# Kernel tuning notes

Measured on AMD Instinct MI355X. Metric: run time of the kernel, lower is better.

The kernel has to match this reference:

```python
import jax, jax.numpy as jnp
import numpy as np

DIM = 2048
N_HEADS = 16
HEAD_DIM = DIM // N_HEADS

def setup_inputs() -> dict:
    key = jax.random.key(0)
    kx, kqkv, kout = jax.random.split(key, 3)
    x = jax.random.normal(kx, (2, 2048, DIM), dtype=jnp.float32)
    # nn.Linear weights stored [out_features, in_features]; y = x @ W.T
    W_qkv = jax.random.normal(kqkv, (3 * DIM, DIM), dtype=jnp.float32) * (DIM ** -0.5)
    W_out = jax.random.normal(kout, (DIM, DIM), dtype=jnp.float32) * (DIM ** -0.5)
    return {"x": x, "W_qkv": W_qkv, "W_out": W_out}

def reference(x, W_qkv, W_out):
    B, T, D = x.shape
    qkv = jnp.einsum('btd,ed->bte', x, W_qkv)  # [B,T,3D]
    q, k, v = jnp.split(qkv, 3, axis=-1)
    def heads(t):
        return t.reshape(B, T, N_HEADS, HEAD_DIM).transpose(0, 2, 1, 3)  # [B,H,T,d]
    q, k, v = heads(q), heads(k), heads(v)
    att = jnp.einsum('bhid,bhjd->bhij', q, k) / (HEAD_DIM ** 0.5)
    causal = jnp.tril(jnp.ones((T, T), dtype=bool))
    att = jnp.where(causal, att, -jnp.inf)
    att = jax.nn.softmax(att, axis=-1)
    out = jnp.einsum('bhij,bhjd->bhid', att, v)
    out = out.transpose(0, 2, 1, 3).reshape(B, T, D)
    return jnp.einsum('btd,ed->bte', out, W_out)
```

## Files before the change

### kernel.cpp

```cpp
#include <hip/hip_runtime.h>

typedef short short8 __attribute__((ext_vector_type(8)));
typedef short short4v __attribute__((ext_vector_type(4)));
typedef float f32x4 __attribute__((ext_vector_type(4)));
typedef unsigned short u16;
typedef u16 ushort4v __attribute__((ext_vector_type(4)));

__device__ inline u16 f2bf(float f){
  unsigned int u = __builtin_bit_cast(unsigned int, f);
  u = (u + 0x7fffu + ((u >> 16) & 1u)) >> 16;
  return (u16)u;
}

__device__ inline short8 cat8(short4v a, short4v b){
  short8 r;
  r[0]=a[0]; r[1]=a[1]; r[2]=a[2]; r[3]=a[3];
  r[4]=b[0]; r[5]=b[1]; r[6]=b[2]; r[7]=b[3];
  return r;
}

__device__ inline void gload_lds16(const void* g, unsigned lds_addr){
  __builtin_amdgcn_global_load_lds((__attribute__((address_space(1))) void*)(uintptr_t)g,
                                   (__attribute__((address_space(3))) void*)(uintptr_t)lds_addr,
                                   16, 0, 0);
}

__global__ void cvt_bf16(const float* __restrict__ in, u16* __restrict__ out, int n4){
  int stride = gridDim.x * blockDim.x;
  for (int i = blockIdx.x * blockDim.x + threadIdx.x; i < n4; i += stride){
    float4 v = ((const float4*)in)[i];
    ushort4v r = { f2bf(v.x), f2bf(v.y), f2bf(v.z), f2bf(v.w) };
    ((ushort4v*)out)[i] = r;
  }
}

template<int OUT_BF16>
__global__ __launch_bounds__(256) void gemm_bt(const u16* __restrict__ A, const u16* __restrict__ B,
                                               void* __restrict__ Cv, int M, int N, int K){
  __shared__ u16 As[128 * 64];
  __shared__ u16 Bs[128 * 64];
  const int tid  = threadIdx.x;
  const int wave = tid >> 6, lane = tid & 63;
  const int lr = lane & 15, lg = lane >> 4;
  const int wm = wave >> 1, wn = wave & 1;
  const long bm = blockIdx.x * 128L, bn = blockIdx.y * 128L;
  const unsigned asb = (unsigned)(uintptr_t)As;
  const unsigned bsb = (unsigned)(uintptr_t)Bs;

  const int  srow = wave * 32 + (lane >> 3);
  const int  scol = ((lane & 7) ^ (lane >> 3)) * 8;
  const u16* aptr = A + (bm + srow) * (long)K + scol;
  const u16* bptr = B + (bn + srow) * (long)K + scol;
  const unsigned sdst = (unsigned)(wave * 4096);

  f32x4 acc[4][4] = {};
  for (int k0 = 0; k0 < K; k0 += 64){
    #pragma unroll
    for (int c = 0; c < 4; c++){
      gload_lds16(aptr + (size_t)(8 * c) * K + k0, asb + sdst + 1024u * c);
      gload_lds16(bptr + (size_t)(8 * c) * K + k0, bsb + sdst + 1024u * c);
    }
    __syncthreads();
    #pragma unroll
    for (int kk = 0; kk < 2; kk++){
      short8 af[4], bfr[4];
      #pragma unroll
      for (int m = 0; m < 4; m++){
        int row = wm * 64 + m * 16 + lr;
        int phys = (kk * 4 + lg) ^ (row & 7);
        af[m] = *(const short8*)&As[row * 64 + phys * 8];
      }
      #pragma unroll
      for (int n = 0; n < 4; n++){
        int row = wn * 64 + n * 16 + lr;
        int phys = (kk * 4 + lg) ^ (row & 7);
        bfr[n] = *(const short8*)&Bs[row * 64 + phys * 8];
      }
      #pragma unroll
      for (int m = 0; m < 4; m++)
        #pragma unroll
        for (int n = 0; n < 4; n++)
          acc[m][n] = __builtin_amdgcn_mfma_f32_16x16x32_bf16(af[m], bfr[n], acc[m][n], 0, 0, 0);
    }
    __syncthreads();
  }
  #pragma unroll
  for (int m = 0; m < 4; m++){
    #pragma unroll
    for (int n = 0; n < 4; n++){
      #pragma unroll
      for (int r = 0; r < 4; r++){
        long row = bm + wm*64 + m*16 + lg*4 + r;
        long col = bn + wn*64 + n*16 + lr;
        float v = acc[m][n][r];
        if (OUT_BF16) ((u16*)Cv)[row * (long)N + col] = f2bf(v);
        else          ((float*)Cv)[row * (long)N + col] = v;
      }
    }
  }
}

__global__ __launch_bounds__(256, 2) void attn_fwd(const u16* __restrict__ qkv, u16* __restrict__ out){
  const int T = 2048, D3 = 6144, D = 2048, HD = 128;
  const int bh = blockIdx.x;
  const int p = blockIdx.y;
  const int b = bh >> 4, h = bh & 15;
  const int tid = threadIdx.x, wave = tid >> 6, lane = tid & 63;
  const int lr = lane & 15, lg = lane >> 4;

  __shared__ u16 Klds[64][136];
  __shared__ u16 Vlds[64][136];
  __shared__ u16 Plds[4][16][72];

  const size_t base = (size_t)b * T * D3;
  const unsigned vtr = (unsigned)(uintptr_t)&Vlds[(lane >> 4) * 8 + ((lane >> 2) & 3)][(lane & 3) * 4];

  const int srow = tid >> 4;
  const int scol = (tid & 15) * 8;
  const u16* kgp = qkv + base + (size_t)srow * D3 + D + h * HD + scol;
  const u16* vgp = kgp + D;

  const int H = 31 - p, L = p;
  const int q0A = H * 64 + wave * 16;
  const int q0B = L * 64 + wave * 16;

  short8 qfA[4], qfB[4];
  {
    const u16* qa = qkv + base + (size_t)(q0A + lr) * D3 + h * HD;
    const u16* qb = qkv + base + (size_t)(q0B + lr) * D3 + h * HD;
    #pragma unroll
    for (int kk = 0; kk < 4; kk++){
      qfA[kk] = *(const short8*)(qa + kk*32 + lg*8);
      qfB[kk] = *(const short8*)(qb + kk*32 + lg*8);
    }
  }

  f32x4 oA[8] = {}, oB[8] = {};
  float mA[4], lA[4], mB[4], lB[4];
  #pragma unroll
  for (int r = 0; r < 4; r++){ mA[r] = -1e30f; lA[r] = 0.f; mB[r] = -1e30f; lB[r] = 0.f; }

  const float scale2 = 0.12751971252971732f;
  const float THR = 11.5f;

  #define PROCESS(QF, O, MR, LW, Q0W, K0) { \
    f32x4 s[4] = {}; \
    _Pragma("unroll") \
    for (int kh = 0; kh < 4; kh++){ \
      _Pragma("unroll") \
      for (int kk = 0; kk < 4; kk++){ \
        short8 kfrag = *(const short8*)&Klds[kh*16 + lr][kk*32 + lg*8]; \
        s[kh] = __builtin_amdgcn_mfma_f32_16x16x32_bf16(QF[kk], kfrag, s[kh], 0, 0, 0); \
      } \
    } \
    const bool need_mask = ((K0) + 63 > (Q0W)); \
    _Pragma("unroll") \
    for (int kh = 0; kh < 4; kh++){ \
      int key = (K0) + kh*16 + lr; \
      _Pragma("unroll") \
      for (int r = 0; r < 4; r++){ \
        float v = s[kh][r] * scale2; \
        if (need_mask && key > (Q0W) + lg*4 + r) v = -1e30f; \
        s[kh][r] = v; \
      } \
    } \
    float mx[4]; \
    _Pragma("unroll") \
    for (int r = 0; r < 4; r++){ \
      float m0 = fmaxf(fmaxf(s[0][r], s[1][r]), fmaxf(s[2][r], s[3][r])); \
      _Pragma("unroll") \
      for (int msk = 8; msk >= 1; msk >>= 1) m0 = fmaxf(m0, __shfl_xor(m0, msk, 64)); \
      mx[r] = m0; \
    } \
    bool cnd = (mx[0] <= MR[0] + THR) && (mx[1] <= MR[1] + THR) && \
               (mx[2] <= MR[2] + THR) && (mx[3] <= MR[3] + THR); \
    if (__all(cnd)){ \
      _Pragma("unroll") \
      for (int r = 0; r < 4; r++){ \
        float p0 = exp2f(s[0][r] - MR[r]); \
        float p1 = exp2f(s[1][r] - MR[r]); \
        float p2 = exp2f(s[2][r] - MR[r]); \
        float p3 = exp2f(s[3][r] - MR[r]); \
        s[0][r] = p0; s[1][r] = p1; s[2][r] = p2; s[3][r] = p3; \
        float rs = (p0 + p1) + (p2 + p3); \
        _Pragma("unroll") \
        for (int msk = 8; msk >= 1; msk >>= 1) rs += __shfl_xor(rs, msk, 64); \
        LW[r] += rs; \
      } \
    } else { \
      float fs[4]; \
      _Pragma("unroll") \
      for (int r = 0; r < 4; r++){ \
        float mnew = fmaxf(MR[r], mx[r]); \
        float f = exp2f(MR[r] - mnew); \
        float p0 = exp2f(s[0][r] - mnew); \
        float p1 = exp2f(s[1][r] - mnew); \
        float p2 = exp2f(s[2][r] - mnew); \
        float p3 = exp2f(s[3][r] - mnew); \
        s[0][r] = p0; s[1][r] = p1; s[2][r] = p2; s[3][r] = p3; \
        float rs = (p0 + p1) + (p2 + p3); \
        _Pragma("unroll") \
        for (int msk = 8; msk >= 1; msk >>= 1) rs += __shfl_xor(rs, msk, 64); \
        LW[r] = LW[r] * f + rs; \
        MR[r] = mnew; \
        fs[r] = f; \
      } \
      _Pragma("unroll") \
      for (int dt = 0; dt < 8; dt++) \
        _Pragma("unroll") \
        for (int r = 0; r < 4; r++) O[dt][r] *= fs[r]; \
    } \
    _Pragma("unroll") \
    for (int kh = 0; kh < 4; kh++) \
      _Pragma("unroll") \
      for (int r = 0; r < 4; r++) \
        Plds[wave][lg*4 + r][kh*16 + lr] = f2bf(s[kh][r]); \
    asm volatile("s_waitcnt lgkmcnt(0)" ::: "memory"); \
    __builtin_amdgcn_sched_barrier(0); \
    short8 pf[2]; \
    _Pragma("unroll") \
    for (int kp2 = 0; kp2 < 2; kp2++) \
      pf[kp2] = *(const short8*)&Plds[wave][lr][kp2*32 + lg*8]; \
    asm volatile("s_waitcnt lgkmcnt(0)" ::: "memory"); \
    __builtin_amdgcn_sched_barrier(0); \
    short4v vf[2][2][2]; \
    asm volatile("ds_read_b64_tr_b16 %0, %1"             : "=v"(vf[0][0][0]) : "v"(vtr)); \
    asm volatile("ds_read_b64_tr_b16 %0, %1 offset:1088" : "=v"(vf[0][0][1]) : "v"(vtr)); \
    asm volatile("ds_read_b64_tr_b16 %0, %1 offset:8704" : "=v"(vf[0][1][0]) : "v"(vtr)); \
    asm volatile("ds_read_b64_tr_b16 %0, %1 offset:9792" : "=v"(vf[0][1][1]) : "v"(vtr)); \
    _Pragma("unroll") \
    for (int dt = 0; dt < 8; dt++){ \
      if (dt < 7){ \
        unsigned pn = vtr + (unsigned)((dt + 1) * 32); \
        int bnx = (dt + 1) & 1; \
        asm volatile("ds_read_b64_tr_b16 %0, %1"             : "=v"(vf[bnx][0][0]) : "v"(pn)); \
        asm volatile("ds_read_b64_tr_b16 %0, %1 offset:1088" : "=v"(vf[bnx][0][1]) : "v"(pn)); \
        asm volatile("ds_read_b64_tr_b16 %0, %1 offset:8704" : "=v"(vf[bnx][1][0]) : "v"(pn)); \
        asm volatile("ds_read_b64_tr_b16 %0, %1 offset:9792" : "=v"(vf[bnx][1][1]) : "v"(pn)); \
        asm volatile("s_waitcnt lgkmcnt(4)" ::: "memory"); \
      } else { \
        asm volatile("s_waitcnt lgkmcnt(0)" ::: "memory"); \
      } \
      __builtin_amdgcn_sched_barrier(0); \
      short8 v0 = cat8(vf[dt & 1][0][0], vf[dt & 1][0][1]); \
      short8 v1 = cat8(vf[dt & 1][1][0], vf[dt & 1][1][1]); \
      O[dt] = __builtin_amdgcn_mfma_f32_16x16x32_bf16(pf[0], v0, O[dt], 0, 0, 0); \
      O[dt] = __builtin_amdgcn_mfma_f32_16x16x32_bf16(pf[1], v1, O[dt], 0, 0, 0); \
    } \
  }

  const int ntiles = H + 1;
  short8 kreg[4], vreg[4];
  #pragma unroll
  for (int c = 0; c < 4; c++){
    kreg[c] = *(const short8*)(kgp + (size_t)(16 * c) * D3);
    vreg[c] = *(const short8*)(vgp + (size_t)(16 * c) * D3);
  }

  for (int t = 0; t < ntiles; t++){
    const int k0 = t * 64;
    __syncthreads();
    #pragma unroll
    for (int c = 0; c < 4; c++){
      *(short8*)&Klds[srow + 16*c][scol] = kreg[c];
      *(short8*)&Vlds[srow + 16*c][scol] = vreg[c];
    }
    __syncthreads();
    if (t + 1 < ntiles){
      const u16* kn = kgp + (size_t)(k0 + 64) * D3;
      const u16* vn = vgp + (size_t)(k0 + 64) * D3;
      #pragma unroll
      for (int c = 0; c < 4; c++){
        kreg[c] = *(const short8*)(kn + (size_t)(16 * c) * D3);
        vreg[c] = *(const short8*)(vn + (size_t)(16 * c) * D3);
      }
    }

    PROCESS(qfA, oA, mA, lA, q0A, k0)
    if (t <= L){
      PROCESS(qfB, oB, mB, lB, q0B, k0)
    }
  }
  #undef PROCESS

  #pragma unroll
  for (int r = 0; r < 4; r++){ lA[r] = 1.0f / lA[r]; lB[r] = 1.0f / lB[r]; }
  #pragma unroll
  for (int dt = 0; dt < 8; dt++){
    #pragma unroll
    for (int r = 0; r < 4; r++){
      int qa = q0A + lg*4 + r;
      out[(size_t)(b * T + qa) * D + h * HD + dt*16 + lr] = f2bf(oA[dt][r] * lA[r]);
      int qb = q0B + lg*4 + r;
      out[(size_t)(b * T + qb) * D + h * HD + dt*16 + lr] = f2bf(oB[dt][r] * lB[r]);
    }
  }
}

extern "C" void kernel_launch(void* const* d_in, const int* in_sizes, int n_in,
                              void* d_out, int out_size, void* d_ws, size_t ws_size,
                              hipStream_t stream) {
  const float* x    = (const float*)d_in[0];
  const float* wqkv = (const float*)d_in[1];
  const float* wout = (const float*)d_in[2];
  float* out = (float*)d_out;

  u16* ws    = (u16*)d_ws;
  u16* xb    = ws;
  u16* wqkvb = xb + 8388608;
  u16* qkvb  = wqkvb + 12582912;
  u16* attnb = xb;
  u16* woutb = wqkvb;

  cvt_bf16<<<2048, 256, 0, stream>>>(x,    xb,    8388608 / 4);
  cvt_bf16<<<2048, 256, 0, stream>>>(wqkv, wqkvb, 12582912 / 4);

  gemm_bt<1><<<dim3(32, 48), 256, 0, stream>>>(xb, wqkvb, qkvb, 4096, 6144, 2048);

  cvt_bf16<<<2048, 256, 0, stream>>>(wout, woutb, 4194304 / 4);

  attn_fwd<<<dim3(32, 16), 256, 0, stream>>>(qkvb, attnb);

  gemm_bt<0><<<dim3(32, 16), 256, 0, stream>>>(attnb, woutb, out, 4096, 2048, 2048);
}
```

Before: 282.0 us.

## Add 256x256 pipelined GEMM for QKV and interleave paired attention tiles

Adds a 512-thread 256x256-tile GEMM that double-buffers LDS using direct global-to-LDS loads, with MFMA priority boosts. It computes the Q and K parts of the QKV projection, while the older 128-tile kernel handles the V columns. The attention kernel now computes the two query tiles' QK and PV MFMAs in one interleaved pass that shares the K and V fragments, using separate P slots in LDS. Attention blocks are also reordered along the y dimension. The intent is to raise data reuse and MFMA density, in exchange for higher register and LDS pressure and two GEMM launches instead of one.

```diff
diff --git a/kernel.cpp b/kernel.cpp
--- a/kernel.cpp
+++ b/kernel.cpp
@@ -34,9 +34,95 @@
   }
 }
 
+#define BARRIER() { __builtin_amdgcn_sched_barrier(0); __builtin_amdgcn_s_barrier(); __builtin_amdgcn_sched_barrier(0); }
+#define VM4() asm volatile("s_waitcnt vmcnt(4)" ::: "memory");
+
+#define MFMA4(MO, AA, BB) { __builtin_amdgcn_s_setprio(1); \
+  _Pragma("unroll") for (int m = 0; m < 4; m++) \
+    _Pragma("unroll") for (int n = 0; n < 4; n++) \
+      acc[(MO)+m][n] = __builtin_amdgcn_mfma_f32_16x16x32_bf16(AA[(MO)+m], BB[n], acc[(MO)+m][n], 0, 0, 0); \
+  __builtin_amdgcn_s_setprio(0); }
+
+#define PHASE4(ABASE, BBASE, ST1, ST2, ST3, ST4) { \
+    const u16* Ab = (ABASE); const u16* Bb = (BBASE); \
+    short8 a0[8], b0[4], a1[8], b1[4]; \
+    _Pragma("unroll") for (int m = 0; m < 8; m++){ int row = wm*128 + m*16 + lr; int ph = lg ^ (row & 7); a0[m] = *(const short8*)&Ab[row*64 + ph*8]; } \
+    _Pragma("unroll") for (int n = 0; n < 4; n++){ int row = wn*64 + n*16 + lr; int ph = lg ^ (row & 7); b0[n] = *(const short8*)&Bb[row*64 + ph*8]; } \
+    ST1 BARRIER() MFMA4(0, a0, b0) BARRIER() \
+    _Pragma("unroll") for (int m = 0; m < 8; m++){ int row = wm*128 + m*16 + lr; int ph = (4+lg) ^ (row & 7); a1[m] = *(const short8*)&Ab[row*64 + ph*8]; } \
+    _Pragma("unroll") for (int n = 0; n < 4; n++){ int row = wn*64 + n*16 + lr; int ph = (4+lg) ^ (row & 7); b1[n] = *(const short8*)&Bb[row*64 + ph*8]; } \
+    ST2 BARRIER() MFMA4(4, a0, b0) BARRIER() \
+    ST3 BARRIER() MFMA4(0, a1, b1) BARRIER() \
+    ST4 VM4() BARRIER() MFMA4(4, a1, b1) BARRIER() \
+  }
+
+template<int OUT_BF16>
+__global__ __launch_bounds__(512, 2) void gemm256(const u16* __restrict__ A, const u16* __restrict__ B,
+                                                  void* __restrict__ Cv, int M, int NS, int K){
+  __shared__ u16 lds[2][32768];
+  const int tid = threadIdx.x, wave = tid >> 6, lane = tid & 63;
+  const int lr = lane & 15, lg = lane >> 4;
+  const int wm = wave >> 2, wn = wave & 3;
+  const long bm = blockIdx.x * 256L, bn = blockIdx.y * 256L;
+  const int l3 = lane >> 3, l7 = lane & 7;
+
+  const u16* asrc = A + (bm + wave*8 + l3) * (long)K + (l7 ^ l3) * 8;
+  const u16* bsrc = B + (bn + wave*8 + l3) * (long)K + (l7 ^ l3) * 8;
+  const unsigned ldsbase = (unsigned)(uintptr_t)&lds[0][0];
+  const unsigned wdst = wave * 1024u;
+
+#define STG_A(BUF,S,KOFF) gload_lds16(asrc + (size_t)(S)*64*K + (KOFF), ldsbase + (BUF)*65536u + wdst + (S)*8192u);
+#define STG_B(BUF,S,KOFF) gload_lds16(bsrc + (size_t)(S)*64*K + (KOFF), ldsbase + (BUF)*65536u + 32768u + wdst + (S)*8192u);
+
+  f32x4 acc[8][4] = {};
+  const int nk = K >> 6;
+
+  #pragma unroll
+  for (int s = 0; s < 4; s++){ STG_A(0, s, 0) }
+  #pragma unroll
+  for (int s = 0; s < 4; s++){ STG_B(0, s, 0) }
+  #pragma unroll
+  for (int s = 0; s < 4; s++){ STG_A(1, s, 64) }
+  VM4()
+  BARRIER()
+
+  for (int i = 0; i < (nk >> 1); i++){
+    const size_t kt1 = (size_t)((2*i + 1) << 6);
+    const size_t kn0 = (size_t)(((2*i + 2) & (nk - 1)) << 6);
+    const size_t kn1 = (size_t)(((2*i + 3) & (nk - 1)) << 6);
+    PHASE4(&lds[0][0], &lds[0][16384],
+           STG_B(1,0,kt1) STG_B(1,1,kt1),
+           STG_B(1,2,kt1) STG_B(1,3,kt1),
+           STG_A(0,0,kn0) STG_A(0,1,kn0),
+           STG_A(0,2,kn0) STG_A(0,3,kn0))
+    PHASE4(&lds[1][0], &lds[1][16384],
+           STG_B(0,0,kn0) STG_B(0,1,kn0),
+           STG_B(0,2,kn0) STG_B(0,3,kn0),
+           STG_A(1,0,kn1) STG_A(1,1,kn1),
+           STG_A(1,2,kn1) STG_A(1,3,kn1))
+  }
+#undef STG_A
+#undef STG_B
+
+  #pragma unroll
+  for (int m = 0; m < 8; m++){
+    #pragma unroll
+    for (int n = 0; n < 4; n++){
+      #pragma unroll
+      for (int r = 0; r < 4; r++){
+        long row = bm + wm*128 + m*16 + lg*4 + r;
+        long col = bn + wn*64 + n*16 + lr;
+        float v = acc[m][n][r];
+        if (OUT_BF16) ((u16*)Cv)[row * (long)NS + col] = f2bf(v);
+        else          ((float*)Cv)[row * (long)NS + col] = v;
+      }
+    }
+  }
+}
+
 template<int OUT_BF16>
 __global__ __launch_bounds__(256) void gemm_bt(const u16* __restrict__ A, const u16* __restrict__ B,
-                                               void* __restrict__ Cv, int M, int N, int K){
+                                               void* __restrict__ Cv, int M, int NS, int K){
   __shared__ u16 As[128 * 64];
   __shared__ u16 Bs[128 * 64];
   const int tid  = threadIdx.x;
@@ -93,8 +179,8 @@
         long row = bm + wm*64 + m*16 + lg*4 + r;
         long col = bn + wn*64 + n*16 + lr;
         float v = acc[m][n][r];
-        if (OUT_BF16) ((u16*)Cv)[row * (long)N + col] = f2bf(v);
-        else          ((float*)Cv)[row * (long)N + col] = v;
+        if (OUT_BF16) ((u16*)Cv)[row * (long)NS + col] = f2bf(v);
+        else          ((float*)Cv)[row * (long)NS + col] = v;
       }
     }
   }
@@ -103,14 +189,15 @@
 __global__ __launch_bounds__(256, 2) void attn_fwd(const u16* __restrict__ qkv, u16* __restrict__ out){
   const int T = 2048, D3 = 6144, D = 2048, HD = 128;
   const int bh = blockIdx.x;
-  const int p = blockIdx.y;
+  const int yy = blockIdx.y;
+  const int p = (yy < 8) ? yy : (23 - yy);
   const int b = bh >> 4, h = bh & 15;
   const int tid = threadIdx.x, wave = tid >> 6, lane = tid & 63;
   const int lr = lane & 15, lg = lane >> 4;
 
   __shared__ u16 Klds[64][136];
   __shared__ u16 Vlds[64][136];
-  __shared__ u16 Plds[4][16][72];
+  __shared__ u16 Plds[8][16][72];
 
   const size_t base = (size_t)b * T * D3;
   const unsigned vtr = (unsigned)(uintptr_t)&Vlds[(lane >> 4) * 8 + ((lane >> 2) & 3)][(lane & 3) * 4];
@@ -143,31 +230,11 @@
   const float scale2 = 0.12751971252971732f;
   const float THR = 11.5f;
 
-  #define PROCESS(QF, O, MR, LW, Q0W, K0) { \
-    f32x4 s[4] = {}; \
-    _Pragma("unroll") \
-    for (int kh = 0; kh < 4; kh++){ \
-      _Pragma("unroll") \
-      for (int kk = 0; kk < 4; kk++){ \
-        short8 kfrag = *(const short8*)&Klds[kh*16 + lr][kk*32 + lg*8]; \
-        s[kh] = __builtin_amdgcn_mfma_f32_16x16x32_bf16(QF[kk], kfrag, s[kh], 0, 0, 0); \
-      } \
-    } \
-    const bool need_mask = ((K0) + 63 > (Q0W)); \
-    _Pragma("unroll") \
-    for (int kh = 0; kh < 4; kh++){ \
-      int key = (K0) + kh*16 + lr; \
-      _Pragma("unroll") \
-      for (int r = 0; r < 4; r++){ \
-        float v = s[kh][r] * scale2; \
-        if (need_mask && key > (Q0W) + lg*4 + r) v = -1e30f; \
-        s[kh][r] = v; \
-      } \
-    } \
+  #define SMAX(S, MR, LW, O, PSLOT) { \
     float mx[4]; \
     _Pragma("unroll") \
     for (int r = 0; r < 4; r++){ \
-      float m0 = fmaxf(fmaxf(s[0][r], s[1][r]), fmaxf(s[2][r], s[3][r])); \
+      float m0 = fmaxf(fmaxf(S[0][r], S[1][r]), fmaxf(S[2][r], S[3][r])); \
       _Pragma("unroll") \
       for (int msk = 8; msk >= 1; msk >>= 1) m0 = fmaxf(m0, __shfl_xor(m0, msk, 64)); \
       mx[r] = m0; \
@@ -177,77 +244,51 @@
     if (__all(cnd)){ \
       _Pragma("unroll") \
       for (int r = 0; r < 4; r++){ \
-        float p0 = exp2f(s[0][r] - MR[r]); \
-        float p1 = exp2f(s[1][r] - MR[r]); \
-        float p2 = exp2f(s[2][r] - MR[r]); \
-        float p3 = exp2f(s[3][r] - MR[r]); \
-        s[0][r] = p0; s[1][r] = p1; s[2][r] = p2; s[3][r] = p3; \
+        float p0 = exp2f(S[0][r] - MR[r]); \
+        float p1 = exp2f(S[1][r] - MR[r]); \
+        float p2 = exp2f(S[2][r] - MR[r]); \
+        float p3 = exp2f(S[3][r] - MR[r]); \
+        S[0][r] = p0; S[1][r] = p1; S[2][r] = p2; S[3][r] = p3; \
         float rs = (p0 + p1) + (p2 + p3); \
         _Pragma("unroll") \
         for (int msk = 8; msk >= 1; msk >>= 1) rs += __shfl_xor(rs, msk, 64); \
         LW[r] += rs; \
       } \
     } else { \
-      float fs[4]; \
+      float fsv[4]; \
       _Pragma("unroll") \
       for (int r = 0; r < 4; r++){ \
         float mnew = fmaxf(MR[r], mx[r]); \
         float f = exp2f(MR[r] - mnew); \
-        float p0 = exp2f(s[0][r] - mnew); \
-        float p1 = exp2f(s[1][r] - mnew); \
-        float p2 = exp2f(s[2][r] - mnew); \
-        float p3 = exp2f(s[3][r] - mnew); \
-        s[0][r] = p0; s[1][r] = p1; s[2][r] = p2; s[3][r] = p3; \
+        float p0 = exp2f(S[0][r] - mnew); \
+        float p1 = exp2f(S[1][r] - mnew); \
+        float p2 = exp2f(S[2][r] - mnew); \
+        float p3 = exp2f(S[3][r] - mnew); \
+        S[0][r] = p0; S[1][r] = p1; S[2][r] = p2; S[3][r] = p3; \
         float rs = (p0 + p1) + (p2 + p3); \
         _Pragma("unroll") \
         for (int msk = 8; msk >= 1; msk >>= 1) rs += __shfl_xor(rs, msk, 64); \
         LW[r] = LW[r] * f + rs; \
         MR[r] = mnew; \
-        fs[r] = f; \
+        fsv[r] = f; \
       } \
       _Pragma("unroll") \
       for (int dt = 0; dt < 8; dt++) \
         _Pragma("unroll") \
-        for (int r = 0; r < 4; r++) O[dt][r] *= fs[r]; \
+        for (int r = 0; r < 4; r++) O[dt][r] *= fsv[r]; \
     } \
     _Pragma("unroll") \
     for (int kh = 0; kh < 4; kh++) \
       _Pragma("unroll") \
       for (int r = 0; r < 4; r++) \
-        Plds[wave][lg*4 + r][kh*16 + lr] = f2bf(s[kh][r]); \
-    asm volatile("s_waitcnt lgkmcnt(0)" ::: "memory"); \
-    __builtin_amdgcn_sched_barrier(0); \
-    short8 pf[2]; \
-    _Pragma("unroll") \
-    for (int kp2 = 0; kp2 < 2; kp2++) \
-      pf[kp2] = *(const short8*)&Plds[wave][lr][kp2*32 + lg*8]; \
-    asm volatile("s_waitcnt lgkmcnt(0)" ::: "memory"); \
-    __builtin_amdgcn_sched_barrier(0); \
-    short4v vf[2][2][2]; \
-    asm volatile("ds_read_b64_tr_b16 %0, %1"             : "=v"(vf[0][0][0]) : "v"(vtr)); \
-    asm volatile("ds_read_b64_tr_b16 %0, %1 offset:1088" : "=v"(vf[0][0][1]) : "v"(vtr)); \
-    asm volatile("ds_read_b64_tr_b16 %0, %1 offset:8704" : "=v"(vf[0][1][0]) : "v"(vtr)); \
-    asm volatile("ds_read_b64_tr_b16 %0, %1 offset:9792" : "=v"(vf[0][1][1]) : "v"(vtr)); \
-    _Pragma("unroll") \
-    for (int dt = 0; dt < 8; dt++){ \
-      if (dt < 7){ \
-        unsigned pn = vtr + (unsigned)((dt + 1) * 32); \
-        int bnx = (dt + 1) & 1; \
-        asm volatile("ds_read_b64_tr_b16 %0, %1"             : "=v"(vf[bnx][0][0]) : "v"(pn)); \
-        asm volatile("ds_read_b64_tr_b16 %0, %1 offset:1088" : "=v"(vf[bnx][0][1]) : "v"(pn)); \
-        asm volatile("ds_read_b64_tr_b16 %0, %1 offset:8704" : "=v"(vf[bnx][1][0]) : "v"(pn)); \
-        asm volatile("ds_read_b64_tr_b16 %0, %1 offset:9792" : "=v"(vf[bnx][1][1]) : "v"(pn)); \
-        asm volatile("s_waitcnt lgkmcnt(4)" ::: "memory"); \
-      } else { \
-        asm volatile("s_waitcnt lgkmcnt(0)" ::: "memory"); \
-      } \
-      __builtin_amdgcn_sched_barrier(0); \
-      short8 v0 = cat8(vf[dt & 1][0][0], vf[dt & 1][0][1]); \
-      short8 v1 = cat8(vf[dt & 1][1][0], vf[dt & 1][1][1]); \
-      O[dt] = __builtin_amdgcn_mfma_f32_16x16x32_bf16(pf[0], v0, O[dt], 0, 0, 0); \
-      O[dt] = __builtin_amdgcn_mfma_f32_16x16x32_bf16(pf[1], v1, O[dt], 0, 0, 0); \
-    } \
-  }
+        Plds[PSLOT][lg*4 + r][kh*16 + lr] = f2bf(S[kh][r]); \
+  }
+
+  #define TR4(VF, BUF, PTR) \
+    asm volatile("ds_read_b64_tr_b16 %0, %1"             : "=v"(VF[BUF][0][0]) : "v"(PTR)); \
+    asm volatile("ds_read_b64_tr_b16 %0, %1 offset:1088" : "=v"(VF[BUF][0][1]) : "v"(PTR)); \
+    asm volatile("ds_read_b64_tr_b16 %0, %1 offset:8704" : "=v"(VF[BUF][1][0]) : "v"(PTR)); \
+    asm volatile("ds_read_b64_tr_b16 %0, %1 offset:9792" : "=v"(VF[BUF][1][1]) : "v"(PTR));
 
   const int ntiles = H + 1;
   short8 kreg[4], vreg[4];
@@ -276,12 +317,111 @@
       }
     }
 
-    PROCESS(qfA, oA, mA, lA, q0A, k0)
     if (t <= L){
-      PROCESS(qfB, oB, mB, lB, q0B, k0)
-    }
-  }
-  #undef PROCESS
+      f32x4 sA[4] = {}, sB[4] = {};
+      #pragma unroll
+      for (int kh = 0; kh < 4; kh++){
+        #pragma unroll
+        for (int kk = 0; kk < 4; kk++){
+          short8 kfrag = *(const short8*)&Klds[kh*16 + lr][kk*32 + lg*8];
+          sA[kh] = __builtin_amdgcn_mfma_f32_16x16x32_bf16(qfA[kk], kfrag, sA[kh], 0, 0, 0);
+          sB[kh] = __builtin_amdgcn_mfma_f32_16x16x32_bf16(qfB[kk], kfrag, sB[kh], 0, 0, 0);
+        }
+      }
+      const bool maskB = (t == L);
+      #pragma unroll
+      for (int kh = 0; kh < 4; kh++){
+        int key = k0 + kh*16 + lr;
+        #pragma unroll
+        for (int r = 0; r < 4; r++){
+          sA[kh][r] *= scale2;
+          float vb = sB[kh][r] * scale2;
+          if (maskB && key > q0B + lg*4 + r) vb = -1e30f;
+          sB[kh][r] = vb;
+        }
+      }
+      SMAX(sA, mA, lA, oA, wave)
+      SMAX(sB, mB, lB, oB, wave + 4)
+      asm volatile("s_waitcnt lgkmcnt(0)" ::: "memory");
+      __builtin_amdgcn_sched_barrier(0);
+      short8 pfA[2], pfB[2];
+      #pragma unroll
+      for (int k2 = 0; k2 < 2; k2++){
+        pfA[k2] = *(const short8*)&Plds[wave][lr][k2*32 + lg*8];
+        pfB[k2] = *(const short8*)&Plds[wave + 4][lr][k2*32 + lg*8];
+      }
+      asm volatile("s_waitcnt lgkmcnt(0)" ::: "memory");
+      __builtin_amdgcn_sched_barrier(0);
+      short4v vf[2][2][2];
+      TR4(vf, 0, vtr)
+      #pragma unroll
+      for (int dt = 0; dt < 8; dt++){
+        if (dt < 7){
+          unsigned pn = vtr + (unsigned)((dt + 1) * 32);
+          TR4(vf, (dt + 1) & 1, pn)
+          asm volatile("s_waitcnt lgkmcnt(4)" ::: "memory");
+        } else {
+          asm volatile("s_waitcnt lgkmcnt(0)" ::: "memory");
+        }
+        __builtin_amdgcn_sched_barrier(0);
+        short8 v0 = cat8(vf[dt & 1][0][0], vf[dt & 1][0][1]);
+        short8 v1 = cat8(vf[dt & 1][1][0], vf[dt & 1][1][1]);
+        oA[dt] = __builtin_amdgcn_mfma_f32_16x16x32_bf16(pfA[0], v0, oA[dt], 0, 0, 0);
+        oB[dt] = __builtin_amdgcn_mfma_f32_16x16x32_bf16(pfB[0], v0, oB[dt], 0, 0, 0);
+        oA[dt] = __builtin_amdgcn_mfma_f32_16x16x32_bf16(pfA[1], v1, oA[dt], 0, 0, 0);
+        oB[dt] = __builtin_amdgcn_mfma_f32_16x16x32_bf16(pfB[1], v1, oB[dt], 0, 0, 0);
+      }
+    } else {
+      f32x4 sA[4] = {};
+      #pragma unroll
+      for (int kh = 0; kh < 4; kh++){
+        #pragma unroll
+        for (int kk = 0; kk < 4; kk++){
+          short8 kfrag = *(const short8*)&Klds[kh*16 + lr][kk*32 + lg*8];
+          sA[kh] = __builtin_amdgcn_mfma_f32_16x16x32_bf16(qfA[kk], kfrag, sA[kh], 0, 0, 0);
+        }
+      }
+      const bool need_mask = (k0 + 63 > q0A);
+      #pragma unroll
+      for (int kh = 0; kh < 4; kh++){
+        int key = k0 + kh*16 + lr;
+        #pragma unroll
+        for (int r = 0; r < 4; r++){
+          float v = sA[kh][r] * scale2;
+          if (need_mask && key > q0A + lg*4 + r) v = -1e30f;
+          sA[kh][r] = v;
+        }
+      }
+      SMAX(sA, mA, lA, oA, wave)
+      asm volatile("s_waitcnt lgkmcnt(0)" ::: "memory");
+      __builtin_amdgcn_sched_barrier(0);
+      short8 pf[2];
+      #pragma unroll
+      for (int k2 = 0; k2 < 2; k2++)
+        pf[k2] = *(const short8*)&Plds[wave][lr][k2*32 + lg*8];
+      asm volatile("s_waitcnt lgkmcnt(0)" ::: "memory");
+      __builtin_amdgcn_sched_barrier(0);
+      short4v vf[2][2][2];
+      TR4(vf, 0, vtr)
+      #pragma unroll
+      for (int dt = 0; dt < 8; dt++){
+        if (dt < 7){
+          unsigned pn = vtr + (unsigned)((dt + 1) * 32);
+          TR4(vf, (dt + 1) & 1, pn)
+          asm volatile("s_waitcnt lgkmcnt(4)" ::: "memory");
+        } else {
+          asm volatile("s_waitcnt lgkmcnt(0)" ::: "memory");
+        }
+        __builtin_amdgcn_sched_barrier(0);
+        short8 v0 = cat8(vf[dt & 1][0][0], vf[dt & 1][0][1]);
+        short8 v1 = cat8(vf[dt & 1][1][0], vf[dt & 1][1][1]);
+        oA[dt] = __builtin_amdgcn_mfma_f32_16x16x32_bf16(pf[0], v0, oA[dt], 0, 0, 0);
+        oA[dt] = __builtin_amdgcn_mfma_f32_16x16x32_bf16(pf[1], v1, oA[dt], 0, 0, 0);
+      }
+    }
+  }
+  #undef SMAX
+  #undef TR4
 
   #pragma unroll
   for (int r = 0; r < 4; r++){ lA[r] = 1.0f / lA[r]; lB[r] = 1.0f / lB[r]; }
@@ -315,7 +455,9 @@
   cvt_bf16<<<2048, 256, 0, stream>>>(x,    xb,    8388608 / 4);
   cvt_bf16<<<2048, 256, 0, stream>>>(wqkv, wqkvb, 12582912 / 4);
 
-  gemm_bt<1><<<dim3(32, 48), 256, 0, stream>>>(xb, wqkvb, qkvb, 4096, 6144, 2048);
+  gemm256<1><<<dim3(16, 16), 512, 0, stream>>>(xb, wqkvb, qkvb, 4096, 6144, 2048);
+  gemm_bt<1><<<dim3(32, 16), 256, 0, stream>>>(xb, wqkvb + (size_t)4096 * 2048,
+                                               qkvb + 4096, 4096, 6144, 2048);
 
   cvt_bf16<<<2048, 256, 0, stream>>>(wout, woutb, 4194304 / 4);
 
```

Measured after the change: 338.8 us. 1.2x slower.
